# Kernel optimization log

Measured on AMD Instinct MI355X. Metric: run time of the kernel, lower is better.

## Reference

```python
import jax, jax.numpy as jnp
import numpy as np

# Synthetic forest: T complete B-ary trees of depth D.
# Nodes stored level-major in `embeds`: level 0 (roots) first, then level 1, ...
# Level l has T*B**l nodes; children of node j at level l are rows j*B..j*B+B-1 of level l+1.
T_TREES, BRANCH, DEPTH = 16, 4, 8
IN_DIM, HIDDEN, N_LABEL = 128, 128, 5


def _level_layout():
    counts = [T_TREES * BRANCH ** l for l in range(DEPTH)]
    offsets = np.concatenate([[0], np.cumsum(counts)]).astype(np.int64)
    return counts, offsets


def setup_inputs() -> dict:
    key = jax.random.key(0)
    counts, offsets = _level_layout()
    n_total = int(offsets[-1])
    ks = jax.random.split(key, 16)
    s_in = 1.0 / np.sqrt(IN_DIM)
    s_h = 1.0 / np.sqrt(HIDDEN)
    d = {"embeds": jax.random.normal(ks[0], (n_total, IN_DIM), dtype=jnp.float32)}
    # gate params: *x linears have bias, *h linears are bias-free (as in torch module)
    d["Wix"] = jax.random.uniform(ks[1], (HIDDEN, IN_DIM), jnp.float32, -s_in, s_in)
    d["bix"] = jax.random.uniform(ks[2], (HIDDEN,), jnp.float32, -s_in, s_in)
    d["Wih"] = jax.random.uniform(ks[3], (HIDDEN, HIDDEN), jnp.float32, -s_h, s_h)
    d["Wfx"] = jax.random.uniform(ks[4], (HIDDEN, IN_DIM), jnp.float32, -s_in, s_in)
    d["bfx"] = jax.random.uniform(ks[5], (HIDDEN,), jnp.float32, -s_in, s_in)
    d["Wfh"] = jax.random.uniform(ks[6], (HIDDEN, HIDDEN), jnp.float32, -s_h, s_h)
    d["Wox"] = jax.random.uniform(ks[7], (HIDDEN, IN_DIM), jnp.float32, -s_in, s_in)
    d["box"] = jax.random.uniform(ks[8], (HIDDEN,), jnp.float32, -s_in, s_in)
    d["Woh"] = jax.random.uniform(ks[9], (HIDDEN, HIDDEN), jnp.float32, -s_h, s_h)
    d["Wux"] = jax.random.uniform(ks[10], (HIDDEN, IN_DIM), jnp.float32, -s_in, s_in)
    d["bux"] = jax.random.uniform(ks[11], (HIDDEN,), jnp.float32, -s_in, s_in)
    d["Wuh"] = jax.random.uniform(ks[12], (HIDDEN, HIDDEN), jnp.float32, -s_h, s_h)
    d["Wout"] = 0.01 * jax.random.normal(ks[13], (N_LABEL, HIDDEN), dtype=jnp.float32)
    d["bout"] = 0.01 * jax.random.normal(ks[14], (N_LABEL,), dtype=jnp.float32)
    return d


def reference(embeds, Wix, bix, Wih, Wfx, bfx, Wfh, Wox, box, Woh, Wux, bux, Wuh, Wout, bout):
    counts, offsets = _level_layout()
    H, B = HIDDEN, BRANCH
    child_h = child_c = None
    # leaves-first (level = DEPTH-1 .. 0), matching `while level >= 0` order
    for level in range(DEPTH - 1, -1, -1):
        n = counts[level]
        o = int(offsets[level])
        x = embeds[o:o + n]  # [n, in_dim] == index_select of this level's nodes
        if child_h is None:  # leaves: zero child state
            h_sum = jnp.zeros((n, H), embeds.dtype)
            fc_sum = jnp.zeros((n, H), embeds.dtype)
        else:
            # child-sum over the B children gathered from the previous level
            h_sum = child_h.reshape(n, B, H).sum(axis=1)  # child_h_sum
            fh = child_h @ Wfh.T  # [n*B, H]
            fx = jnp.repeat(x, B, axis=0) @ Wfx.T + bfx  # parent embed per child
            f = jax.nn.sigmoid(fx + fh)
            fc_sum = (f * child_c).reshape(n, B, H).sum(axis=1)  # child_fc_sum
        i = jax.nn.sigmoid(x @ Wix.T + bix + h_sum @ Wih.T)
        og = jax.nn.sigmoid(x @ Wox.T + box + h_sum @ Woh.T)
        u = jnp.tanh(x @ Wux.T + bux + h_sum @ Wuh.T)
        c = i * u + fc_sum
        h = og * jnp.tanh(c)
        child_c, child_h = c, h
    # output head at the root level (dropout is identity at eval)
    return child_h @ Wout.T + bout  # [T_TREES, N_LABEL]
```

## Files before the change

kernel.cpp:

```cpp
#include <hip/hip_runtime.h>
#include <hip/hip_bf16.h>


#define HID 128

typedef unsigned short u16;
typedef unsigned int u32;
typedef __attribute__((ext_vector_type(8))) short short8;
typedef __attribute__((ext_vector_type(4))) float floatx4;

__device__ __forceinline__ float bf2f(u16 u) {
  union { unsigned int u; float f; } v; v.u = ((unsigned int)u) << 16; return v.f;
}
__device__ __forceinline__ u16 f2bf(float f) {
  __hip_bfloat16 b = __float2bfloat16(f);
  return *reinterpret_cast<u16*>(&b);
}
__device__ __forceinline__ short8 f2bf8(float4 f0, float4 f1) {
  short8 s;
  s[0] = (short)f2bf(f0.x); s[1] = (short)f2bf(f0.y);
  s[2] = (short)f2bf(f0.z); s[3] = (short)f2bf(f0.w);
  s[4] = (short)f2bf(f1.x); s[5] = (short)f2bf(f1.y);
  s[6] = (short)f2bf(f1.z); s[7] = (short)f2bf(f1.w);
  return s;
}
__device__ __forceinline__ float sigm(float x) {
  return __builtin_amdgcn_rcpf(1.0f + __expf(-x));
}
__device__ __forceinline__ float tanh_fast(float x) {
  float ax = fabsf(x);
  float e = __expf(2.0f * ax);
  float t = 1.0f - 2.0f * __builtin_amdgcn_rcpf(e + 1.0f);
  return copysignf(t, x);
}

__global__ void prep_weights(const float* __restrict__ Wix, const float* __restrict__ Wih,
                             const float* __restrict__ Wfx, const float* __restrict__ Wfh,
                             const float* __restrict__ Wox, const float* __restrict__ Woh,
                             const float* __restrict__ Wux, const float* __restrict__ Wuh,
                             u16* __restrict__ Wcat, u16* __restrict__ Wfxb, u16* __restrict__ Wfhb)
{
  int t = blockIdx.x * 256 + threadIdx.x;
  if (t < 98304) {
    int nrow = t >> 8, k = t & 255;
    int gate = nrow >> 7, r = nrow & 127;
    float v;
    if (k < 128) {
      const float* W = (gate == 0) ? Wix : (gate == 1) ? Wox : Wux;
      v = W[r * 128 + k];
    } else {
      const float* W = (gate == 0) ? Wih : (gate == 1) ? Woh : Wuh;
      v = W[r * 128 + (k - 128)];
    }
    Wcat[t] = f2bf(v);
  } else if (t < 98304 + 16384) {
    int i = t - 98304;
    Wfxb[i] = f2bf(Wfx[i]);
  } else if (t < 98304 + 32768) {
    int i = t - 98304 - 16384;
    Wfhb[i] = f2bf(Wfh[i]);
  }
}

template <int MODE>
__global__ __launch_bounds__(512, 2)
void tree_kernel(const float* __restrict__ embeds,
                 const u16* __restrict__ Wcat,
                 const u16* __restrict__ Wfxb,
                 const u16* __restrict__ Wfhb,
                 const float* __restrict__ bix, const float* __restrict__ bfx,
                 const float* __restrict__ box, const float* __restrict__ bux,
                 u16* __restrict__ hf, u32* __restrict__ cf_buf,
                 int n, int noff, int coff, int poff)
{
  constexpr bool HASC = (MODE >= 1);
  constexpr bool ROOT = (MODE == 2);
  extern __shared__ char smem[];
  u16* sx  = (u16*)smem;
  u16* shs = (u16*)(smem + 16384);

  const int tid  = threadIdx.x;
  const int wave = tid >> 6;
  const int lane = tid & 63;
  const int lg   = lane >> 4;
  const int ln   = lane & 15;
  const int pbase = blockIdx.x * 64;
  const int col  = wave * 16 + ln;

  {
    int row = tid >> 3;
    int k0  = (tid & 7) * 16;
    const float* src = embeds + (size_t)(noff + pbase + row) * HID + k0;
    unsigned sw = ((unsigned)(row & 7)) << 4;
    char* dst = (char*)sx + row * 256;
    float4 f0 = *(const float4*)src;
    float4 f1 = *(const float4*)(src + 4);
    float4 f2 = *(const float4*)(src + 8);
    float4 f3 = *(const float4*)(src + 12);
    *(short8*)(dst + (((unsigned)(k0 * 2)) ^ sw))      = f2bf8(f0, f1);
    *(short8*)(dst + (((unsigned)(k0 * 2 + 16)) ^ sw)) = f2bf8(f2, f3);
  }

  if constexpr (HASC) {
    int row = tid >> 3, cg = tid & 7;
    const u16* src = hf + (size_t)(noff + pbase + row) * HID + cg * 16;
    short8 v0 = *(const short8*)src;
    short8 v1 = *(const short8*)(src + 8);
    unsigned sw = ((unsigned)(row & 7)) << 4;
    char* dst = (char*)shs + row * 256;
    *(short8*)(dst + ((cg * 32) ^ sw))      = v0;
    *(short8*)(dst + ((cg * 32 + 16) ^ sw)) = v1;
  }

  __syncthreads();

  float fc[4][4];
  if constexpr (HASC) {
    floatx4 accx[4] = {};
#pragma unroll
    for (int kt = 0; kt < 4; ++kt) {
      short8 b = *(const short8*)(Wfxb + (size_t)(wave * 16 + ln) * HID + kt * 32 + lg * 8);
#pragma unroll
      for (int m = 0; m < 4; ++m) {
        int row = m * 16 + ln;
        unsigned sw = ((unsigned)(row & 7)) << 4;
        short8 a = *(const short8*)((char*)sx + row * 256 +
                                    (((unsigned)((kt * 32 + lg * 8) * 2)) ^ sw));
        accx[m] = __builtin_amdgcn_mfma_f32_16x16x32_bf16(a, b, accx[m], 0, 0, 0);
      }
    }
    float bf = bfx[col];
#pragma unroll
    for (int m = 0; m < 4; ++m) {
      u32 cf[4][4];
#pragma unroll
      for (int r = 0; r < 4; ++r) {
        int row = m * 16 + lg * 4 + r;
        size_t cb = (size_t)(coff + 4 * (pbase + row)) * HID + col;
#pragma unroll
        for (int k = 0; k < 4; ++k)
          cf[r][k] = cf_buf[cb + (size_t)k * HID];
      }
#pragma unroll
      for (int r = 0; r < 4; ++r) {
        float fxv = accx[m][r] + bf;
        float s = 0.f;
#pragma unroll
        for (int k = 0; k < 4; ++k) {
          float fhv = bf2f((u16)(cf[r][k] & 0xFFFFu));
          float cv  = bf2f((u16)(cf[r][k] >> 16));
          s += sigm(fxv + fhv) * cv;
        }
        fc[m][r] = s;
      }
    }
  }

  floatx4 acc[4][3] = {};
  constexpr int KT = HASC ? 8 : 4;
#pragma unroll
  for (int kt = 0; kt < KT; ++kt) {
    short8 a[4];
#pragma unroll
    for (int m = 0; m < 4; ++m) {
      int row = m * 16 + ln;
      unsigned sw = ((unsigned)(row & 7)) << 4;
      const char* base = (kt < 4) ? (const char*)sx : (const char*)shs;
      int kb = ((kt & 3) * 32 + lg * 8) * 2;
      a[m] = *(const short8*)(base + row * 256 + (((unsigned)kb) ^ sw));
    }
#pragma unroll
    for (int g = 0; g < 3; ++g) {
      short8 b = *(const short8*)(Wcat + (size_t)((g * 8 + wave) * 16 + ln) * 256 + kt * 32 + lg * 8);
#pragma unroll
      for (int m = 0; m < 4; ++m)
        acc[m][g] = __builtin_amdgcn_mfma_f32_16x16x32_bf16(a[m], b, acc[m][g], 0, 0, 0);
    }
  }

  __syncthreads();

  u16 cbf[4][4];
  {
    float bi = bix[col], bo = box[col], bu = bux[col];
#pragma unroll
    for (int m = 0; m < 4; ++m) {
      float hs4 = 0.f;
#pragma unroll
      for (int r = 0; r < 4; ++r) {
        int row = m * 16 + lg * 4 + r;
        bool ok = ROOT ? (pbase + row < n) : true;
        if (ok) {
          float iv = sigm(acc[m][0][r] + bi);
          float ov = sigm(acc[m][1][r] + bo);
          float uv = tanh_fast(acc[m][2][r] + bu);
          float fcv = HASC ? fc[m][r] : 0.f;
          float cv = iv * uv + fcv;
          float hv = ov * tanh_fast(cv);
          if constexpr (ROOT) {
            hf[(size_t)(noff + pbase + row) * HID + col] = f2bf(hv);
          } else {
            cbf[m][r] = f2bf(cv);
            hs4 += hv;
            unsigned sw = ((unsigned)(row & 7)) << 4;
            *(u16*)((char*)sx + row * 256 + (((unsigned)(col * 2)) ^ sw)) = f2bf(hv);
          }
        }
      }
      if constexpr (!ROOT)
        hf[(size_t)(poff + (pbase >> 2) + m * 4 + lg) * HID + col] = f2bf(hs4);
    }
  }

  if constexpr (!ROOT) {
    __syncthreads();
    floatx4 ah[4] = {};
#pragma unroll
    for (int kt = 0; kt < 4; ++kt) {
      short8 b = *(const short8*)(Wfhb + (size_t)(wave * 16 + ln) * HID + kt * 32 + lg * 8);
#pragma unroll
      for (int m = 0; m < 4; ++m) {
        int row = m * 16 + ln;
        unsigned sw = ((unsigned)(row & 7)) << 4;
        short8 a = *(const short8*)((char*)sx + row * 256 +
                                    (((unsigned)((kt * 32 + lg * 8) * 2)) ^ sw));
        ah[m] = __builtin_amdgcn_mfma_f32_16x16x32_bf16(a, b, ah[m], 0, 0, 0);
      }
    }
#pragma unroll
    for (int m = 0; m < 4; ++m)
#pragma unroll
      for (int r = 0; r < 4; ++r) {
        int row = m * 16 + lg * 4 + r;
        u32 packed = ((u32)cbf[m][r] << 16) | (u32)f2bf(ah[m][r]);
        cf_buf[(size_t)(noff + pbase + row) * HID + col] = packed;
      }
  }
}

__global__ void out_kernel(const u16* __restrict__ hf, const float* __restrict__ Wout,
                           const float* __restrict__ bout, float* __restrict__ out)
{
  int t = threadIdx.x;
  if (t < 80) {
    int row = t / 5, lbl = t - row * 5;
    float s = bout[lbl];
    for (int k = 0; k < 128; ++k)
      s += bf2f(hf[row * 128 + k]) * Wout[lbl * 128 + k];
    out[t] = s;
  }
}

extern "C" void kernel_launch(void* const* d_in, const int* in_sizes, int n_in,
                              void* d_out, int out_size, void* d_ws, size_t ws_size,
                              hipStream_t stream)
{
  const float* embeds = (const float*)d_in[0];
  const float* Wix = (const float*)d_in[1];
  const float* bix = (const float*)d_in[2];
  const float* Wih = (const float*)d_in[3];
  const float* Wfx = (const float*)d_in[4];
  const float* bfx = (const float*)d_in[5];
  const float* Wfh = (const float*)d_in[6];
  const float* Wox = (const float*)d_in[7];
  const float* box = (const float*)d_in[8];
  const float* Woh = (const float*)d_in[9];
  const float* Wux = (const float*)d_in[10];
  const float* bux = (const float*)d_in[11];
  const float* Wuh = (const float*)d_in[12];
  const float* Wout = (const float*)d_in[13];
  const float* bout = (const float*)d_in[14];

  static const int counts[8]  = {16, 64, 256, 1024, 4096, 16384, 65536, 262144};
  static const int offsets[9] = {0, 16, 80, 336, 1360, 5456, 21840, 87376, 349520};

  char* ws = (char*)d_ws;
  u16* hf     = (u16*)ws;
  u32* cf_buf = (u32*)(ws + 89477120);
  u16* Wcat   = (u16*)(ws + 89477120 + 178954240);
  u16* Wfxb   = Wcat + 384 * 256;
  u16* Wfhb   = Wfxb + 128 * 128;

  prep_weights<<<512, 256, 0, stream>>>(Wix, Wih, Wfx, Wfh, Wox, Woh, Wux, Wuh,
                                        Wcat, Wfxb, Wfhb);

  tree_kernel<0><<<262144 / 64, 512, 16384, stream>>>(
      embeds, Wcat, Wfxb, Wfhb, bix, bfx, box, bux,
      hf, cf_buf, 262144, 87376, 0, 21840);

  for (int l = 6; l >= 1; --l) {
    int n = counts[l];
    tree_kernel<1><<<n / 64, 512, 32768, stream>>>(
        embeds, Wcat, Wfxb, Wfhb, bix, bfx, box, bux,
        hf, cf_buf, n, offsets[l], offsets[l + 1], offsets[l - 1]);
  }

  tree_kernel<2><<<1, 512, 32768, stream>>>(
      embeds, Wcat, Wfxb, Wfhb, bix, bfx, box, bux,
      hf, cf_buf, 16, 0, 16, 0);

  out_kernel<<<1, 128, 0, stream>>>(hf, Wout, bout, (float*)d_out);
}
```

Measured before the change: 289.6 us.

## Fuse top tree levels and output head into one per-tree kernel

Levels 3 through 0 and the output projection now run in a single kernel with one block per tree, looping over levels inside the block. This replaces five tiny launches, each using very few blocks. The template kernel is split into dedicated leaf and level kernels with static shared memory. The fused path reads embeds and hidden rows past each tree's valid range when a level has fewer than 64 nodes, and masks the stores. At level 0 it also reads cf_buf rows that belong to other trees, which may be benign or may not.

New measurement: 303.0 us. 1.05x slower.

```diff
diff --git a/kernel.cpp b/kernel.cpp
--- a/kernel.cpp
+++ b/kernel.cpp
@@ -62,22 +62,17 @@
   }
 }
 
-template <int MODE>
 __global__ __launch_bounds__(512, 2)
-void tree_kernel(const float* __restrict__ embeds,
+void leaf_kernel(const float* __restrict__ embeds,
                  const u16* __restrict__ Wcat,
-                 const u16* __restrict__ Wfxb,
                  const u16* __restrict__ Wfhb,
-                 const float* __restrict__ bix, const float* __restrict__ bfx,
-                 const float* __restrict__ box, const float* __restrict__ bux,
+                 const float* __restrict__ bix, const float* __restrict__ box,
+                 const float* __restrict__ bux,
                  u16* __restrict__ hf, u32* __restrict__ cf_buf,
-                 int n, int noff, int coff, int poff)
+                 int noff, int poff)
 {
-  constexpr bool HASC = (MODE >= 1);
-  constexpr bool ROOT = (MODE == 2);
-  extern __shared__ char smem[];
-  u16* sx  = (u16*)smem;
-  u16* shs = (u16*)(smem + 16384);
+  __shared__ char smem[16384];
+  u16* sx = (u16*)smem;
 
   const int tid  = threadIdx.x;
   const int wave = tid >> 6;
@@ -101,7 +96,111 @@
     *(short8*)(dst + (((unsigned)(k0 * 2 + 16)) ^ sw)) = f2bf8(f2, f3);
   }
 
-  if constexpr (HASC) {
+  const float bi = bix[col], bo = box[col], bu = bux[col];
+  __syncthreads();
+
+  floatx4 acc[4][3] = {};
+#pragma unroll
+  for (int kt = 0; kt < 4; ++kt) {
+    short8 a[4];
+#pragma unroll
+    for (int m = 0; m < 4; ++m) {
+      int row = m * 16 + ln;
+      unsigned sw = ((unsigned)(row & 7)) << 4;
+      a[m] = *(const short8*)((char*)sx + row * 256 +
+                              (((unsigned)((kt * 32 + lg * 8) * 2)) ^ sw));
+    }
+#pragma unroll
+    for (int g = 0; g < 3; ++g) {
+      short8 b = *(const short8*)(Wcat + (size_t)((g * 8 + wave) * 16 + ln) * 256 + kt * 32 + lg * 8);
+#pragma unroll
+      for (int m = 0; m < 4; ++m)
+        acc[m][g] = __builtin_amdgcn_mfma_f32_16x16x32_bf16(a[m], b, acc[m][g], 0, 0, 0);
+    }
+  }
+
+  __syncthreads();
+
+  u16 cbf[4][4];
+#pragma unroll
+  for (int m = 0; m < 4; ++m) {
+    float hs4 = 0.f;
+#pragma unroll
+    for (int r = 0; r < 4; ++r) {
+      int row = m * 16 + lg * 4 + r;
+      float iv = sigm(acc[m][0][r] + bi);
+      float ov = sigm(acc[m][1][r] + bo);
+      float uv = tanh_fast(acc[m][2][r] + bu);
+      float cv = iv * uv;
+      float hv = ov * tanh_fast(cv);
+      cbf[m][r] = f2bf(cv);
+      hs4 += hv;
+      unsigned sw = ((unsigned)(row & 7)) << 4;
+      *(u16*)((char*)sx + row * 256 + (((unsigned)(col * 2)) ^ sw)) = f2bf(hv);
+    }
+    hf[(size_t)(poff + (pbase >> 2) + m * 4 + lg) * HID + col] = f2bf(hs4);
+  }
+
+  __syncthreads();
+  floatx4 ah[4] = {};
+#pragma unroll
+  for (int kt = 0; kt < 4; ++kt) {
+    short8 b = *(const short8*)(Wfhb + (size_t)(wave * 16 + ln) * HID + kt * 32 + lg * 8);
+#pragma unroll
+    for (int m = 0; m < 4; ++m) {
+      int row = m * 16 + ln;
+      unsigned sw = ((unsigned)(row & 7)) << 4;
+      short8 a = *(const short8*)((char*)sx + row * 256 +
+                                  (((unsigned)((kt * 32 + lg * 8) * 2)) ^ sw));
+      ah[m] = __builtin_amdgcn_mfma_f32_16x16x32_bf16(a, b, ah[m], 0, 0, 0);
+    }
+  }
+#pragma unroll
+  for (int m = 0; m < 4; ++m)
+#pragma unroll
+    for (int r = 0; r < 4; ++r) {
+      int row = m * 16 + lg * 4 + r;
+      u32 packed = ((u32)cbf[m][r] << 16) | (u32)f2bf(ah[m][r]);
+      cf_buf[(size_t)(noff + pbase + row) * HID + col] = packed;
+    }
+}
+
+__global__ __launch_bounds__(512, 2)
+void level_kernel(const float* __restrict__ embeds,
+                  const u16* __restrict__ Wcat,
+                  const u16* __restrict__ Wfxb,
+                  const u16* __restrict__ Wfhb,
+                  const float* __restrict__ bix, const float* __restrict__ bfx,
+                  const float* __restrict__ box, const float* __restrict__ bux,
+                  u16* __restrict__ hf, u32* __restrict__ cf_buf,
+                  int noff, int coff, int poff)
+{
+  __shared__ char smem[32768];
+  u16* sx  = (u16*)smem;
+  u16* shs = (u16*)(smem + 16384);
+
+  const int tid  = threadIdx.x;
+  const int wave = tid >> 6;
+  const int lane = tid & 63;
+  const int lg   = lane >> 4;
+  const int ln   = lane & 15;
+  const int pbase = blockIdx.x * 64;
+  const int col  = wave * 16 + ln;
+
+  {
+    int row = tid >> 3;
+    int k0  = (tid & 7) * 16;
+    const float* src = embeds + (size_t)(noff + pbase + row) * HID + k0;
+    unsigned sw = ((unsigned)(row & 7)) << 4;
+    char* dst = (char*)sx + row * 256;
+    float4 f0 = *(const float4*)src;
+    float4 f1 = *(const float4*)(src + 4);
+    float4 f2 = *(const float4*)(src + 8);
+    float4 f3 = *(const float4*)(src + 12);
+    *(short8*)(dst + (((unsigned)(k0 * 2)) ^ sw))      = f2bf8(f0, f1);
+    *(short8*)(dst + (((unsigned)(k0 * 2 + 16)) ^ sw)) = f2bf8(f2, f3);
+  }
+  {
     int row = tid >> 3, cg = tid & 7;
     const u16* src = hf + (size_t)(noff + pbase + row) * HID + cg * 16;
     short8 v0 = *(const short8*)src;
@@ -111,11 +210,10 @@
     *(short8*)(dst + ((cg * 32) ^ sw))      = v0;
     *(short8*)(dst + ((cg * 32 + 16) ^ sw)) = v1;
   }
-
   __syncthreads();
 
   float fc[4][4];
-  if constexpr (HASC) {
+  {
     floatx4 accx[4] = {};
 #pragma unroll
     for (int kt = 0; kt < 4; ++kt) {
@@ -157,9 +255,8 @@
   }
 
   floatx4 acc[4][3] = {};
-  constexpr int KT = HASC ? 8 : 4;
-#pragma unroll
-  for (int kt = 0; kt < KT; ++kt) {
+#pragma unroll
+  for (int kt = 0; kt < 8; ++kt) {
     short8 a[4];
 #pragma unroll
     for (int m = 0; m < 4; ++m) {
@@ -177,7 +274,6 @@
         acc[m][g] = __builtin_amdgcn_mfma_f32_16x16x32_bf16(a[m], b, acc[m][g], 0, 0, 0);
     }
   }
-
   __syncthreads();
 
   u16 cbf[4][4];
@@ -189,65 +285,228 @@
 #pragma unroll
       for (int r = 0; r < 4; ++r) {
         int row = m * 16 + lg * 4 + r;
-        bool ok = ROOT ? (pbase + row < n) : true;
-        if (ok) {
-          float iv = sigm(acc[m][0][r] + bi);
-          float ov = sigm(acc[m][1][r] + bo);
-          float uv = tanh_fast(acc[m][2][r] + bu);
-          float fcv = HASC ? fc[m][r] : 0.f;
-          float cv = iv * uv + fcv;
-          float hv = ov * tanh_fast(cv);
-          if constexpr (ROOT) {
-            hf[(size_t)(noff + pbase + row) * HID + col] = f2bf(hv);
-          } else {
-            cbf[m][r] = f2bf(cv);
-            hs4 += hv;
-            unsigned sw = ((unsigned)(row & 7)) << 4;
-            *(u16*)((char*)sx + row * 256 + (((unsigned)(col * 2)) ^ sw)) = f2bf(hv);
+        float iv = sigm(acc[m][0][r] + bi);
+        float ov = sigm(acc[m][1][r] + bo);
+        float uv = tanh_fast(acc[m][2][r] + bu);
+        float cv = iv * uv + fc[m][r];
+        float hv = ov * tanh_fast(cv);
+        cbf[m][r] = f2bf(cv);
+        hs4 += hv;
+        unsigned sw = ((unsigned)(row & 7)) << 4;
+        *(u16*)((char*)sx + row * 256 + (((unsigned)(col * 2)) ^ sw)) = f2bf(hv);
+      }
+      hf[(size_t)(poff + (pbase >> 2) + m * 4 + lg) * HID + col] = f2bf(hs4);
+    }
+  }
+
+  __syncthreads();
+  floatx4 ah[4] = {};
+#pragma unroll
+  for (int kt = 0; kt < 4; ++kt) {
+    short8 b = *(const short8*)(Wfhb + (size_t)(wave * 16 + ln) * HID + kt * 32 + lg * 8);
+#pragma unroll
+    for (int m = 0; m < 4; ++m) {
+      int row = m * 16 + ln;
+      unsigned sw = ((unsigned)(row & 7)) << 4;
+      short8 a = *(const short8*)((char*)sx + row * 256 +
+                                  (((unsigned)((kt * 32 + lg * 8) * 2)) ^ sw));
+      ah[m] = __builtin_amdgcn_mfma_f32_16x16x32_bf16(a, b, ah[m], 0, 0, 0);
+    }
+  }
+#pragma unroll
+  for (int m = 0; m < 4; ++m)
+#pragma unroll
+    for (int r = 0; r < 4; ++r) {
+      int row = m * 16 + lg * 4 + r;
+      u32 packed = ((u32)cbf[m][r] << 16) | (u32)f2bf(ah[m][r]);
+      cf_buf[(size_t)(noff + pbase + row) * HID + col] = packed;
+    }
+}
+
+__global__ __launch_bounds__(512, 2)
+void fused_small(const float* __restrict__ embeds,
+                 const u16* __restrict__ Wcat,
+                 const u16* __restrict__ Wfxb,
+                 const u16* __restrict__ Wfhb,
+                 const float* __restrict__ bix, const float* __restrict__ bfx,
+                 const float* __restrict__ box, const float* __restrict__ bux,
+                 const float* __restrict__ Wout, const float* __restrict__ bout,
+                 u16* __restrict__ hf, u32* __restrict__ cf_buf,
+                 float* __restrict__ out)
+{
+  __shared__ char smem[32768];
+  u16* sx  = (u16*)smem;
+  u16* shs = (u16*)(smem + 16384);
+
+  const int tid  = threadIdx.x;
+  const int wave = tid >> 6;
+  const int lane = tid & 63;
+  const int lg   = lane >> 4;
+  const int ln   = lane & 15;
+  const int col  = wave * 16 + ln;
+  const int t    = blockIdx.x;
+
+  const int offs[5] = {0, 16, 80, 336, 1360};
+  const int cpt[5]  = {1, 4, 16, 64, 256};
+
+#pragma unroll 1
+  for (int l = 3; l >= 0; --l) {
+    const int nrows = cpt[l];
+    const int noff  = offs[l] + t * cpt[l];
+    const int coff  = offs[l + 1] + t * cpt[l + 1];
+    const int poff  = (l > 0) ? offs[l - 1] + t * cpt[l - 1] : 0;
+
+    {
+      int row = tid >> 3;
+      int k0  = (tid & 7) * 16;
+      const float* src = embeds + (size_t)(noff + row) * HID + k0;
+      unsigned sw = ((unsigned)(row & 7)) << 4;
+      char* dst = (char*)sx + row * 256;
+      float4 f0 = *(const float4*)src;
+      float4 f1 = *(const float4*)(src + 4);
+      float4 f2 = *(const float4*)(src + 8);
+      float4 f3 = *(const float4*)(src + 12);
+      *(short8*)(dst + (((unsigned)(k0 * 2)) ^ sw))      = f2bf8(f0, f1);
+      *(short8*)(dst + (((unsigned)(k0 * 2 + 16)) ^ sw)) = f2bf8(f2, f3);
+    }
+    {
+      int row = tid >> 3, cg = tid & 7;
+      const u16* src = hf + (size_t)(noff + row) * HID + cg * 16;
+      short8 v0 = *(const short8*)src;
+      short8 v1 = *(const short8*)(src + 8);
+      unsigned sw = ((unsigned)(row & 7)) << 4;
+      char* dst = (char*)shs + row * 256;
+      *(short8*)(dst + ((cg * 32) ^ sw))      = v0;
+      *(short8*)(dst + ((cg * 32 + 16) ^ sw)) = v1;
+    }
+    __syncthreads();
+
+    float fc[4][4];
+    {
+      floatx4 accx[4] = {};
+#pragma unroll
+      for (int kt = 0; kt < 4; ++kt) {
+        short8 b = *(const short8*)(Wfxb + (size_t)(wave * 16 + ln) * HID + kt * 32 + lg * 8);
+#pragma unroll
+        for (int m = 0; m < 4; ++m) {
+          int row = m * 16 + ln;
+          unsigned sw = ((unsigned)(row & 7)) << 4;
+          short8 a = *(const short8*)((char*)sx + row * 256 +
+                                      (((unsigned)((kt * 32 + lg * 8) * 2)) ^ sw));
+          accx[m] = __builtin_amdgcn_mfma_f32_16x16x32_bf16(a, b, accx[m], 0, 0, 0);
+        }
+      }
+      float bf = bfx[col];
+#pragma unroll
+      for (int m = 0; m < 4; ++m) {
+        u32 cf[4][4];
+#pragma unroll
+        for (int r = 0; r < 4; ++r) {
+          int row = m * 16 + lg * 4 + r;
+          size_t cb = (size_t)(coff + 4 * row) * HID + col;
+#pragma unroll
+          for (int k = 0; k < 4; ++k)
+            cf[r][k] = cf_buf[cb + (size_t)k * HID];
+        }
+#pragma unroll
+        for (int r = 0; r < 4; ++r) {
+          float fxv = accx[m][r] + bf;
+          float s = 0.f;
+#pragma unroll
+          for (int k = 0; k < 4; ++k) {
+            float fhv = bf2f((u16)(cf[r][k] & 0xFFFFu));
+            float cv  = bf2f((u16)(cf[r][k] >> 16));
+            s += sigm(fxv + fhv) * cv;
           }
-        }
-      }
-      if constexpr (!ROOT)
-        hf[(size_t)(poff + (pbase >> 2) + m * 4 + lg) * HID + col] = f2bf(hs4);
-    }
-  }
-
-  if constexpr (!ROOT) {
-    __syncthreads();
-    floatx4 ah[4] = {};
-#pragma unroll
-    for (int kt = 0; kt < 4; ++kt) {
-      short8 b = *(const short8*)(Wfhb + (size_t)(wave * 16 + ln) * HID + kt * 32 + lg * 8);
+          fc[m][r] = s;
+        }
+      }
+    }
+
+    floatx4 acc[4][3] = {};
+#pragma unroll
+    for (int kt = 0; kt < 8; ++kt) {
+      short8 a[4];
 #pragma unroll
       for (int m = 0; m < 4; ++m) {
         int row = m * 16 + ln;
         unsigned sw = ((unsigned)(row & 7)) << 4;
-        short8 a = *(const short8*)((char*)sx + row * 256 +
-                                    (((unsigned)((kt * 32 + lg * 8) * 2)) ^ sw));
-        ah[m] = __builtin_amdgcn_mfma_f32_16x16x32_bf16(a, b, ah[m], 0, 0, 0);
-      }
-    }
-#pragma unroll
-    for (int m = 0; m < 4; ++m)
-#pragma unroll
-      for (int r = 0; r < 4; ++r) {
-        int row = m * 16 + lg * 4 + r;
-        u32 packed = ((u32)cbf[m][r] << 16) | (u32)f2bf(ah[m][r]);
-        cf_buf[(size_t)(noff + pbase + row) * HID + col] = packed;
-      }
-  }
-}
-
-__global__ void out_kernel(const u16* __restrict__ hf, const float* __restrict__ Wout,
-                           const float* __restrict__ bout, float* __restrict__ out)
-{
-  int t = threadIdx.x;
-  if (t < 80) {
-    int row = t / 5, lbl = t - row * 5;
-    float s = bout[lbl];
+        const char* base = (kt < 4) ? (const char*)sx : (const char*)shs;
+        int kb = ((kt & 3) * 32 + lg * 8) * 2;
+        a[m] = *(const short8*)(base + row * 256 + (((unsigned)kb) ^ sw));
+      }
+#pragma unroll
+      for (int g = 0; g < 3; ++g) {
+        short8 b = *(const short8*)(Wcat + (size_t)((g * 8 + wave) * 16 + ln) * 256 + kt * 32 + lg * 8);
+#pragma unroll
+        for (int m = 0; m < 4; ++m)
+          acc[m][g] = __builtin_amdgcn_mfma_f32_16x16x32_bf16(a[m], b, acc[m][g], 0, 0, 0);
+      }
+    }
+    __syncthreads();
+
+    u16 cbf[4][4];
+    {
+      float bi = bix[col], bo = box[col], bu = bux[col];
+#pragma unroll
+      for (int m = 0; m < 4; ++m) {
+        float hs4 = 0.f;
+#pragma unroll
+        for (int r = 0; r < 4; ++r) {
+          int row = m * 16 + lg * 4 + r;
+          if (row < nrows) {
+            float iv = sigm(acc[m][0][r] + bi);
+            float ov = sigm(acc[m][1][r] + bo);
+            float uv = tanh_fast(acc[m][2][r] + bu);
+            float cv = iv * uv + fc[m][r];
+            float hv = ov * tanh_fast(cv);
+            unsigned sw = ((unsigned)(row & 7)) << 4;
+            *(u16*)((char*)sx + row * 256 + (((unsigned)(col * 2)) ^ sw)) = f2bf(hv);
+            if (l > 0) { cbf[m][r] = f2bf(cv); hs4 += hv; }
+          }
+        }
+        if (l > 0 && (m * 4 + lg) < (nrows >> 2))
+          hf[(size_t)(poff + m * 4 + lg) * HID + col] = f2bf(hs4);
+      }
+    }
+
+    if (l > 0) {
+      __syncthreads();
+      floatx4 ah[4] = {};
+#pragma unroll
+      for (int kt = 0; kt < 4; ++kt) {
+        short8 b = *(const short8*)(Wfhb + (size_t)(wave * 16 + ln) * HID + kt * 32 + lg * 8);
+#pragma unroll
+        for (int m = 0; m < 4; ++m) {
+          int row = m * 16 + ln;
+          unsigned sw = ((unsigned)(row & 7)) << 4;
+          short8 a = *(const short8*)((char*)sx + row * 256 +
+                                      (((unsigned)((kt * 32 + lg * 8) * 2)) ^ sw));
+          ah[m] = __builtin_amdgcn_mfma_f32_16x16x32_bf16(a, b, ah[m], 0, 0, 0);
+        }
+      }
+#pragma unroll
+      for (int m = 0; m < 4; ++m)
+#pragma unroll
+        for (int r = 0; r < 4; ++r) {
+          int row = m * 16 + lg * 4 + r;
+          if (row < nrows) {
+            u32 packed = ((u32)cbf[m][r] << 16) | (u32)f2bf(ah[m][r]);
+            cf_buf[(size_t)(noff + row) * HID + col] = packed;
+          }
+        }
+    }
+    __syncthreads();
+  }
+
+  if (tid < 5) {
+    float s = bout[tid];
+    const u16* hrow = sx;
+    const float* wr = Wout + tid * 128;
+#pragma unroll 4
     for (int k = 0; k < 128; ++k)
-      s += bf2f(hf[row * 128 + k]) * Wout[lbl * 128 + k];
-    out[t] = s;
+      s += bf2f(hrow[k]) * wr[k];
+    out[t * 5 + tid] = s;
   }
 }
 
@@ -271,9 +530,6 @@
   const float* Wout = (const float*)d_in[13];
   const float* bout = (const float*)d_in[14];
 
-  static const int counts[8]  = {16, 64, 256, 1024, 4096, 16384, 65536, 262144};
-  static const int offsets[9] = {0, 16, 80, 336, 1360, 5456, 21840, 87376, 349520};
-
   char* ws = (char*)d_ws;
   u16* hf     = (u16*)ws;
   u32* cf_buf = (u32*)(ws + 89477120);
@@ -284,20 +540,16 @@
   prep_weights<<<512, 256, 0, stream>>>(Wix, Wih, Wfx, Wfh, Wox, Woh, Wux, Wuh,
                                         Wcat, Wfxb, Wfhb);
 
-  tree_kernel<0><<<262144 / 64, 512, 16384, stream>>>(
-      embeds, Wcat, Wfxb, Wfhb, bix, bfx, box, bux,
-      hf, cf_buf, 262144, 87376, 0, 21840);
-
-  for (int l = 6; l >= 1; --l) {
-    int n = counts[l];
-    tree_kernel<1><<<n / 64, 512, 32768, stream>>>(
-        embeds, Wcat, Wfxb, Wfhb, bix, bfx, box, bux,
-        hf, cf_buf, n, offsets[l], offsets[l + 1], offsets[l - 1]);
-  }
-
-  tree_kernel<2><<<1, 512, 32768, stream>>>(
-      embeds, Wcat, Wfxb, Wfhb, bix, bfx, box, bux,
-      hf, cf_buf, 16, 0, 16, 0);
-
-  out_kernel<<<1, 128, 0, stream>>>(hf, Wout, bout, (float*)d_out);
-}
+  leaf_kernel<<<262144 / 64, 512, 0, stream>>>(
+      embeds, Wcat, Wfhb, bix, box, bux, hf, cf_buf, 87376, 21840);
+
+  level_kernel<<<1024, 512, 0, stream>>>(embeds, Wcat, Wfxb, Wfhb, bix, bfx, box, bux,
+                                         hf, cf_buf, 21840, 87376, 5456);
+  level_kernel<<<256, 512, 0, stream>>>(embeds, Wcat, Wfxb, Wfhb, bix, bfx, box, bux,
+                                        hf, cf_buf, 5456, 21840, 1360);
+  level_kernel<<<64, 512, 0, stream>>>(embeds, Wcat, Wfxb, Wfhb, bix, bfx, box, bux,
+                                       hf, cf_buf, 1360, 5456, 336);
+
+  fused_small<<<16, 512, 0, stream>>>(embeds, Wcat, Wfxb, Wfhb, bix, bfx, box, bux,
+                                      Wout, bout, hf, cf_buf, (float*)d_out);
+}
```
